# Kernel optimization log

Measured on AMD Instinct MI355X. Metric: run time of the kernel, lower is better.

## Reference

```python
import jax, jax.numpy as jnp
import numpy as np

OFFSET_BOUND = 8.0


def _bilinear_sample(img, py, px):
    """Bilinear sample with zero padding outside the image.
    img: [N,C,H,W]; py, px: [N,Ho,Wo] float coords. Returns [N,Ho,Wo,C]."""
    N, C, H, W = img.shape
    y0f = jnp.floor(py)
    x0f = jnp.floor(px)
    ly = py - y0f
    lx = px - x0f
    y0 = y0f.astype(jnp.int32)
    x0 = x0f.astype(jnp.int32)
    b = jnp.arange(N, dtype=jnp.int32)[:, None, None]

    def gather(yi, xi):
        valid = (yi >= 0) & (yi < H) & (xi >= 0) & (xi < W)
        yc = jnp.clip(yi, 0, H - 1)
        xc = jnp.clip(xi, 0, W - 1)
        v = img[b, :, yc, xc]  # [N,Ho,Wo,C]
        return v * valid[..., None].astype(img.dtype)

    w00 = ((1.0 - ly) * (1.0 - lx))[..., None]
    w01 = ((1.0 - ly) * lx)[..., None]
    w10 = (ly * (1.0 - lx))[..., None]
    w11 = (ly * lx)[..., None]
    return (gather(y0, x0) * w00 + gather(y0, x0 + 1) * w01 +
            gather(y0 + 1, x0) * w10 + gather(y0 + 1, x0 + 1) * w11)


def setup_inputs() -> dict:
    key = jax.random.key(0)
    k1, k2, k3, k4, k5 = jax.random.split(key, 5)
    N, Cin, Cout, H, W = 8, 64, 64, 256, 256
    x = jax.random.normal(k1, (N, Cin, H, W), dtype=jnp.float32)
    # 1x1 point-wise conv weight, stored as [Cout, Cin]
    pw_weight = jax.random.normal(k2, (Cout, Cin), dtype=jnp.float32) * (1.0 / np.sqrt(Cin))
    # offset-scale predictor (1x1 conv, deformable_groups=1). Module inits to 0;
    # we use small random values so the deformable gather is exercised.
    off_weight = jax.random.normal(k3, (1, Cout), dtype=jnp.float32) * 0.1
    off_bias = jax.random.normal(k4, (1,), dtype=jnp.float32) * 0.1
    # depthwise 3x3 weight [Cout, 3, 3] (groups = Cout, so 1 input channel each)
    dw_weight = jax.random.normal(k5, (Cout, 3, 3), dtype=jnp.float32) * (1.0 / 3.0)
    return {"x": x, "pw_weight": pw_weight, "off_weight": off_weight,
            "off_bias": off_bias, "dw_weight": dw_weight}


def reference(x, pw_weight, off_weight, off_bias, dw_weight):
    # 1x1 point-wise conv
    y = jnp.einsum('nchw,oc->nohw', x, pw_weight)  # [N,Cout,H,W]
    # per-pixel offset scale s, clamped to [0, offset_bound]
    s = jnp.einsum('nchw,dc->ndhw', y, off_weight) + off_bias[None, :, None, None]
    s = jnp.clip(s, 0.0, OFFSET_BOUND)[:, 0]  # [N,H,W] (deformable_groups=1)

    N, C, H, W = y.shape
    ii = jnp.arange(H, dtype=y.dtype)[None, :, None]  # output row index
    jj = jnp.arange(W, dtype=y.dtype)[None, None, :]  # output col index

    # deform_conv with stride=1, pad=1, dil=1; offset = template(dy,dx) * s
    out = jnp.zeros((N, H, W, C), dtype=y.dtype)
    for k in range(9):
        ky, kx = k // 3, k % 3
        dy, dx = float(ky - 1), float(kx - 1)
        py = ii - 1.0 + ky + dy * s  # [N,H,W]
        px = jj - 1.0 + kx + dx * s
        samp = _bilinear_sample(y, py, px)  # [N,H,W,C]
        out = out + samp * dw_weight[:, ky, kx]  # depthwise tap weight per C
    return jnp.transpose(out, (0, 3, 1, 2))  # [N,C,H,W]
```

## Files before the change

### kernel.cpp

```cpp
#include <hip/hip_runtime.h>
#include <hip/hip_fp16.h>
#include <stdint.h>

#define H_   256
#define W_   256
#define HW_  65536
#define NIMG 8

#define TI   32
#define TJ   64
#define HALO 10
#define RDI  52
#define RDJ  84

typedef _Float16 half8_t __attribute__((ext_vector_type(8)));
typedef __fp16   fp16x2  __attribute__((ext_vector_type(2)));
typedef float    float4_t __attribute__((ext_vector_type(4)));

__device__ __forceinline__ uint32_t pk2(float a, float b) {
    fp16x2 h = __builtin_amdgcn_cvt_pkrtz(a, b);
    union { fp16x2 h; uint32_t u; } v; v.h = h; return v.u;
}
__device__ __forceinline__ __half2 u2h(uint32_t u) {
    union { uint32_t u; __half2 h; } v; v.u = u; return v.h;
}
__device__ __forceinline__ __half2 lerp2(__half2 p, __half2 q, __half2 f) {
    return __hfma2(f, __hsub2(q, p), p);
}

__global__ __launch_bounds__(256) void pw_off_kernel(
    const float* __restrict__ x, const float* __restrict__ pw,
    const float* __restrict__ offw, const float* __restrict__ offb,
    uint32_t* __restrict__ ypackI, float* __restrict__ sbuf)
{
    const int t    = threadIdx.x;
    const int blk  = blockIdx.x;
    const int n    = blk >> 8;
    const int hw0  = (blk & 255) << 8;
    const int lane = t & 63;
    const int l15  = lane & 15;
    const int q    = lane >> 4;
    const int wv   = t >> 6;

    half8_t af[4][2];
    #pragma unroll
    for (int mt = 0; mt < 4; ++mt) {
        #pragma unroll
        for (int kt = 0; kt < 2; ++kt) {
            const float* wr = pw + (mt * 16 + l15) * 64 + kt * 32 + q * 8;
            float4 w0 = *(const float4*)wr;
            float4 w1 = *(const float4*)(wr + 4);
            union { uint32_t u[4]; half8_t h; } v;
            v.u[0] = pk2(w0.x, w0.y); v.u[1] = pk2(w0.z, w0.w);
            v.u[2] = pk2(w1.x, w1.y); v.u[3] = pk2(w1.z, w1.w);
            af[mt][kt] = v.h;
        }
    }
    float4_t ow4[4];
    #pragma unroll
    for (int mt = 0; mt < 4; ++mt)
        ow4[mt] = *(const float4_t*)(offw + mt * 16 + q * 4);
    const float bias = offb[0];

    #pragma unroll
    for (int j = 0; j < 4; ++j) {
        const int pix = (wv * 4 + j) * 16 + l15;
        const int hw  = hw0 + pix;
        const float* xp = x + (size_t)n * 64 * HW_ + hw;

        half8_t bf[2];
        #pragma unroll
        for (int kt = 0; kt < 2; ++kt) {
            const float* xk = xp + (size_t)(kt * 32 + q * 8) * HW_;
            float v0 = xk[0 * (size_t)HW_];
            float v1 = xk[1 * (size_t)HW_];
            float v2 = xk[2 * (size_t)HW_];
            float v3 = xk[3 * (size_t)HW_];
            float v4 = xk[4 * (size_t)HW_];
            float v5 = xk[5 * (size_t)HW_];
            float v6 = xk[6 * (size_t)HW_];
            float v7 = xk[7 * (size_t)HW_];
            union { uint32_t u[4]; half8_t h; } vv;
            vv.u[0] = pk2(v0, v1); vv.u[1] = pk2(v2, v3);
            vv.u[2] = pk2(v4, v5); vv.u[3] = pk2(v6, v7);
            bf[kt] = vv.h;
        }

        float4_t acc[4] = {{0,0,0,0},{0,0,0,0},{0,0,0,0},{0,0,0,0}};
        #pragma unroll
        for (int kt = 0; kt < 2; ++kt) {
            #pragma unroll
            for (int mt = 0; mt < 4; ++mt)
                acc[mt] = __builtin_amdgcn_mfma_f32_16x16x32_f16(af[mt][kt], bf[kt], acc[mt], 0, 0, 0);
        }

        float sp = 0.f;
        #pragma unroll
        for (int mt = 0; mt < 4; ++mt)
            sp += acc[mt][0] * ow4[mt][0] + acc[mt][1] * ow4[mt][1]
                + acc[mt][2] * ow4[mt][2] + acc[mt][3] * ow4[mt][3];
        sp += __shfl_xor(sp, 16, 64);
        sp += __shfl_xor(sp, 32, 64);
        float sv = fminf(fmaxf(sp + bias, 0.f), 8.f);
        if (q == 0) sbuf[(size_t)n * HW_ + hw] = sv;

        #pragma unroll
        for (int mt = 0; mt < 4; ++mt) {
            uint2 st;
            st.x = pk2(acc[mt][0], acc[mt][1]);
            st.y = pk2(acc[mt][2], acc[mt][3]);
            const int pg = mt * 2 + (q >> 1);
            size_t ad = (((size_t)(n * 8 + pg)) * HW_ + hw) * 4 + (q & 1) * 2;
            *(uint2*)&ypackI[ad] = st;
        }
    }
}

__global__ __launch_bounds__(512) void deform_kernel(
    const uint4* __restrict__ ypackI, const float* __restrict__ sbuf,
    const float* __restrict__ dwp, float* __restrict__ out)
{
    __shared__ uint4 smem[RDI * RDJ];

    const int t  = threadIdx.x;
    const int tj = blockIdx.x;
    const int ti = blockIdx.y;
    const int z  = blockIdx.z;
    const int n  = z >> 3;
    const int pg = z & 7;
    const int i0 = ti * TI, j0 = tj * TJ;

    const size_t ybase = (size_t)z * HW_;
    uint4 vst[9];
    #pragma unroll
    for (int u = 0; u < 9; ++u) {
        const int idx = t + u * 512;
        uint4 v = {0u, 0u, 0u, 0u};
        if (u < 8 || t < RDI * RDJ - 8 * 512) {
            int r  = idx / RDJ;
            int c  = idx - r * RDJ;
            int gr = i0 - HALO + r;
            int gc = j0 - HALO + c;
            bool ok = (gr >= 0) & (gr < H_) & (gc >= 0) & (gc < W_);
            if (ok) v = ypackI[ybase + gr * W_ + gc];
        }
        vst[u] = v;
    }
    #pragma unroll
    for (int u = 0; u < 9; ++u) {
        const int idx = t + u * 512;
        if (u < 8 || t < RDI * RDJ - 8 * 512)
            smem[idx] = vst[u];
    }

    const int c0 = pg * 8;
    __half2 d2[4][9];
    #pragma unroll
    for (int pp = 0; pp < 4; ++pp) {
        #pragma unroll
        for (int k = 0; k < 9; ++k)
            d2[pp][k] = __floats2half2_rn(dwp[(c0 + 2 * pp) * 9 + k],
                                          dwp[(c0 + 2 * pp + 1) * 9 + k]);
    }
    __syncthreads();

    const int lj = t & 63;
    const int l8 = t >> 6;

    #pragma unroll
    for (int qq = 0; qq < 4; ++qq) {
        const int li = l8 + qq * 8;
        const int gi = i0 + li, gj = j0 + lj;
        const float sv = sbuf[(size_t)n * HW_ + gi * W_ + gj];
        const float tt = 1.0f + sv;
        const float lr = (float)(li + HALO);
        const float lc = (float)(lj + HALO);
        const int ra0 = (int)floorf(lr - tt); const float fya = (lr - tt) - (float)ra0;
        const int rb0 = (int)floorf(lr + tt); const float fyb = (lr + tt) - (float)rb0;
        const int ca0 = (int)floorf(lc - tt); const float fxa = (lc - tt) - (float)ca0;
        const int cb0 = (int)floorf(lc + tt); const float fxb = (lc + tt) - (float)cb0;
        const int rc = li + HALO, cc = lj + HALO;
        const __half2 fxa2 = __float2half2_rn(fxa);
        const __half2 fxb2 = __float2half2_rn(fxb);
        const __half2 fya2 = __float2half2_rn(fya);
        const __half2 fyb2 = __float2half2_rn(fyb);

        __half2 A0[4], C0[4], B0[4], A1[4], C1[4], B1[4];

#define LOADCOLS(ro, Av, Cv, Bv) do {                                   \
        uint4 v0 = smem[(ro) + ca0]; uint4 v1 = smem[(ro) + ca0 + 1];   \
        uint4 vc = smem[(ro) + cc];                                     \
        uint4 v3 = smem[(ro) + cb0]; uint4 v4 = smem[(ro) + cb0 + 1];   \
        const uint32_t* p0 = (const uint32_t*)&v0;                      \
        const uint32_t* p1 = (const uint32_t*)&v1;                      \
        const uint32_t* pc = (const uint32_t*)&vc;                      \
        const uint32_t* p3 = (const uint32_t*)&v3;                      \
        const uint32_t* p4 = (const uint32_t*)&v4;                      \
        _Pragma("unroll")                                               \
        for (int pp = 0; pp < 4; ++pp) {                                \
            Av[pp] = lerp2(u2h(p0[pp]), u2h(p1[pp]), fxa2);             \
            Cv[pp] = u2h(pc[pp]);                                       \
            Bv[pp] = lerp2(u2h(p3[pp]), u2h(p4[pp]), fxb2);             \
        } } while (0)

        __half2 acc[4];
        LOADCOLS(ra0 * RDJ, A0, C0, B0);
        LOADCOLS((ra0 + 1) * RDJ, A1, C1, B1);
        #pragma unroll
        for (int pp = 0; pp < 4; ++pp) {
            __half2 SA = lerp2(A0[pp], A1[pp], fya2);
            __half2 SC = lerp2(C0[pp], C1[pp], fya2);
            __half2 SB = lerp2(B0[pp], B1[pp], fya2);
            acc[pp] = __hmul2(d2[pp][0], SA);
            acc[pp] = __hfma2(d2[pp][1], SC, acc[pp]);
            acc[pp] = __hfma2(d2[pp][2], SB, acc[pp]);
        }
        LOADCOLS(rc * RDJ, A0, C0, B0);
        #pragma unroll
        for (int pp = 0; pp < 4; ++pp) {
            acc[pp] = __hfma2(d2[pp][3], A0[pp], acc[pp]);
            acc[pp] = __hfma2(d2[pp][4], C0[pp], acc[pp]);
            acc[pp] = __hfma2(d2[pp][5], B0[pp], acc[pp]);
        }
        LOADCOLS(rb0 * RDJ, A0, C0, B0);
        LOADCOLS((rb0 + 1) * RDJ, A1, C1, B1);
        #pragma unroll
        for (int pp = 0; pp < 4; ++pp) {
            __half2 SA = lerp2(A0[pp], A1[pp], fyb2);
            __half2 SC = lerp2(C0[pp], C1[pp], fyb2);
            __half2 SB = lerp2(B0[pp], B1[pp], fyb2);
            acc[pp] = __hfma2(d2[pp][6], SA, acc[pp]);
            acc[pp] = __hfma2(d2[pp][7], SC, acc[pp]);
            acc[pp] = __hfma2(d2[pp][8], SB, acc[pp]);
        }
#undef LOADCOLS

        const size_t ob = ((size_t)n * 64 + c0) * HW_ + gi * W_ + gj;
        #pragma unroll
        for (int pp = 0; pp < 4; ++pp) {
            out[ob + (size_t)(2 * pp) * HW_]     = __low2float(acc[pp]);
            out[ob + (size_t)(2 * pp + 1) * HW_] = __high2float(acc[pp]);
        }
    }
}

extern "C" void kernel_launch(void* const* d_in, const int* in_sizes, int n_in,
                              void* d_out, int out_size, void* d_ws, size_t ws_size,
                              hipStream_t stream) {
    const float* x    = (const float*)d_in[0];
    const float* pw   = (const float*)d_in[1];
    const float* offw = (const float*)d_in[2];
    const float* offb = (const float*)d_in[3];
    const float* dwp  = (const float*)d_in[4];

    uint32_t* ypackI = (uint32_t*)d_ws;
    float* sbuf = (float*)((char*)d_ws + (size_t)NIMG * 8 * HW_ * 16);
    float* out  = (float*)d_out;

    hipLaunchKernelGGL(pw_off_kernel, dim3(2048), dim3(256), 0, stream,
                       x, pw, offw, offb, ypackI, sbuf);
    hipLaunchKernelGGL(deform_kernel, dim3(4, 8, NIMG * 8), dim3(512), 0, stream,
                       (const uint4*)ypackI, sbuf, dwp, out);
}
```

Baseline: 285.8 us.

## Remap deform blocks across XCDs, skip zero-weight bilinear loads, split accumulators

Grid becomes 1D with a swizzle that spreads consecutive tiles across the 8 XCDs for L2 locality. Halo staging changes from a register-buffered unrolled load to a simple strided loop. When s is clamped to 0 or 8 the fractional weights are zero, so the second LDS reads of each bilinear pair are skipped under a per-pixel predicate. The three tap-row sums use separate accumulators to shorten dependency chains, at the cost of divergence and a few more registers.

New measurement: 303.7 us. 6.2% more time.

```diff
diff --git a/kernel.cpp b/kernel.cpp
--- a/kernel.cpp
+++ b/kernel.cpp
@@ -123,34 +123,25 @@
     __shared__ uint4 smem[RDI * RDJ];
 
     const int t  = threadIdx.x;
-    const int tj = blockIdx.x;
-    const int ti = blockIdx.y;
-    const int z  = blockIdx.z;
+    const int b  = blockIdx.x;
+    const int sb = (b & 7) * 256 + (b >> 3);
+    const int z  = sb >> 5;
+    const int ti = (sb >> 2) & 7;
+    const int tj = sb & 3;
     const int n  = z >> 3;
     const int pg = z & 7;
     const int i0 = ti * TI, j0 = tj * TJ;
 
     const size_t ybase = (size_t)z * HW_;
-    uint4 vst[9];
-    #pragma unroll
-    for (int u = 0; u < 9; ++u) {
-        const int idx = t + u * 512;
+    for (int idx = t; idx < RDI * RDJ; idx += 512) {
+        int r  = idx / RDJ;
+        int c  = idx - r * RDJ;
+        int gr = i0 - HALO + r;
+        int gc = j0 - HALO + c;
+        bool ok = (gr >= 0) & (gr < H_) & (gc >= 0) & (gc < W_);
         uint4 v = {0u, 0u, 0u, 0u};
-        if (u < 8 || t < RDI * RDJ - 8 * 512) {
-            int r  = idx / RDJ;
-            int c  = idx - r * RDJ;
-            int gr = i0 - HALO + r;
-            int gc = j0 - HALO + c;
-            bool ok = (gr >= 0) & (gr < H_) & (gc >= 0) & (gc < W_);
-            if (ok) v = ypackI[ybase + gr * W_ + gc];
-        }
-        vst[u] = v;
-    }
-    #pragma unroll
-    for (int u = 0; u < 9; ++u) {
-        const int idx = t + u * 512;
-        if (u < 8 || t < RDI * RDJ - 8 * 512)
-            smem[idx] = vst[u];
+        if (ok) v = ypackI[ybase + gr * W_ + gc];
+        smem[idx] = v;
     }
 
     const int c0 = pg * 8;
@@ -172,6 +163,7 @@
         const int li = l8 + qq * 8;
         const int gi = i0 + li, gj = j0 + lj;
         const float sv = sbuf[(size_t)n * HW_ + gi * W_ + gj];
+        const bool act = (sv > 0.0f) & (sv < 8.0f);
         const float tt = 1.0f + sv;
         const float lr = (float)(li + HALO);
         const float lc = (float)(lj + HALO);
@@ -187,10 +179,17 @@
 
         __half2 A0[4], C0[4], B0[4], A1[4], C1[4], B1[4];
 
-#define LOADCOLS(ro, Av, Cv, Bv) do {                                   \
-        uint4 v0 = smem[(ro) + ca0]; uint4 v1 = smem[(ro) + ca0 + 1];   \
-        uint4 vc = smem[(ro) + cc];                                     \
-        uint4 v3 = smem[(ro) + cb0]; uint4 v4 = smem[(ro) + cb0 + 1];   \
+#define LOADCOLS(ro, ALW, Av, Cv, Bv) do {                              \
+        uint4 v0 = {0u,0u,0u,0u}, v1 = {0u,0u,0u,0u}, vc = {0u,0u,0u,0u}; \
+        uint4 v3 = {0u,0u,0u,0u}, v4 = {0u,0u,0u,0u};                   \
+        if (ALW) {                                                      \
+            v0 = smem[(ro) + ca0]; vc = smem[(ro) + cc]; v3 = smem[(ro) + cb0]; \
+            if (act) { v1 = smem[(ro) + ca0 + 1]; v4 = smem[(ro) + cb0 + 1]; } \
+        } else if (act) {                                               \
+            v0 = smem[(ro) + ca0]; v1 = smem[(ro) + ca0 + 1];           \
+            vc = smem[(ro) + cc];                                       \
+            v3 = smem[(ro) + cb0]; v4 = smem[(ro) + cb0 + 1];           \
+        }                                                               \
         const uint32_t* p0 = (const uint32_t*)&v0;                      \
         const uint32_t* p1 = (const uint32_t*)&v1;                      \
         const uint32_t* pc = (const uint32_t*)&vc;                      \
@@ -203,43 +202,44 @@
             Bv[pp] = lerp2(u2h(p3[pp]), u2h(p4[pp]), fxb2);             \
         } } while (0)
 
-        __half2 acc[4];
-        LOADCOLS(ra0 * RDJ, A0, C0, B0);
-        LOADCOLS((ra0 + 1) * RDJ, A1, C1, B1);
+        __half2 t0[4], t1[4], t2[4];
+        LOADCOLS(ra0 * RDJ, 1, A0, C0, B0);
+        LOADCOLS((ra0 + 1) * RDJ, 0, A1, C1, B1);
         #pragma unroll
         for (int pp = 0; pp < 4; ++pp) {
             __half2 SA = lerp2(A0[pp], A1[pp], fya2);
             __half2 SC = lerp2(C0[pp], C1[pp], fya2);
             __half2 SB = lerp2(B0[pp], B1[pp], fya2);
-            acc[pp] = __hmul2(d2[pp][0], SA);
-            acc[pp] = __hfma2(d2[pp][1], SC, acc[pp]);
-            acc[pp] = __hfma2(d2[pp][2], SB, acc[pp]);
-        }
-        LOADCOLS(rc * RDJ, A0, C0, B0);
-        #pragma unroll
-        for (int pp = 0; pp < 4; ++pp) {
-            acc[pp] = __hfma2(d2[pp][3], A0[pp], acc[pp]);
-            acc[pp] = __hfma2(d2[pp][4], C0[pp], acc[pp]);
-            acc[pp] = __hfma2(d2[pp][5], B0[pp], acc[pp]);
-        }
-        LOADCOLS(rb0 * RDJ, A0, C0, B0);
-        LOADCOLS((rb0 + 1) * RDJ, A1, C1, B1);
+            t0[pp] = __hmul2(d2[pp][0], SA);
+            t0[pp] = __hfma2(d2[pp][1], SC, t0[pp]);
+            t0[pp] = __hfma2(d2[pp][2], SB, t0[pp]);
+        }
+        LOADCOLS(rc * RDJ, 1, A0, C0, B0);
+        #pragma unroll
+        for (int pp = 0; pp < 4; ++pp) {
+            t1[pp] = __hmul2(d2[pp][3], A0[pp]);
+            t1[pp] = __hfma2(d2[pp][4], C0[pp], t1[pp]);
+            t1[pp] = __hfma2(d2[pp][5], B0[pp], t1[pp]);
+        }
+        LOADCOLS(rb0 * RDJ, 1, A0, C0, B0);
+        LOADCOLS((rb0 + 1) * RDJ, 0, A1, C1, B1);
         #pragma unroll
         for (int pp = 0; pp < 4; ++pp) {
             __half2 SA = lerp2(A0[pp], A1[pp], fyb2);
             __half2 SC = lerp2(C0[pp], C1[pp], fyb2);
             __half2 SB = lerp2(B0[pp], B1[pp], fyb2);
-            acc[pp] = __hfma2(d2[pp][6], SA, acc[pp]);
-            acc[pp] = __hfma2(d2[pp][7], SC, acc[pp]);
-            acc[pp] = __hfma2(d2[pp][8], SB, acc[pp]);
+            t2[pp] = __hmul2(d2[pp][6], SA);
+            t2[pp] = __hfma2(d2[pp][7], SC, t2[pp]);
+            t2[pp] = __hfma2(d2[pp][8], SB, t2[pp]);
         }
 #undef LOADCOLS
 
         const size_t ob = ((size_t)n * 64 + c0) * HW_ + gi * W_ + gj;
         #pragma unroll
         for (int pp = 0; pp < 4; ++pp) {
-            out[ob + (size_t)(2 * pp) * HW_]     = __low2float(acc[pp]);
-            out[ob + (size_t)(2 * pp + 1) * HW_] = __high2float(acc[pp]);
+            __half2 acc = __hadd2(__hadd2(t0[pp], t1[pp]), t2[pp]);
+            out[ob + (size_t)(2 * pp) * HW_]     = __low2float(acc);
+            out[ob + (size_t)(2 * pp + 1) * HW_] = __high2float(acc);
         }
     }
 }
@@ -259,6 +259,6 @@
 
     hipLaunchKernelGGL(pw_off_kernel, dim3(2048), dim3(256), 0, stream,
                        x, pw, offw, offb, ypackI, sbuf);
-    hipLaunchKernelGGL(deform_kernel, dim3(4, 8, NIMG * 8), dim3(512), 0, stream,
+    hipLaunchKernelGGL(deform_kernel, dim3(2048), dim3(512), 0, stream,
                        (const uint4*)ypackI, sbuf, dwp, out);
 }
```
